# Kernel tuning notes

Hardware: AMD Instinct MI355X
Metric: run time of the kernel (lower is better)

Reference implementation:

```python
import jax, jax.numpy as jnp
import numpy as np

PATCH_LEN = 25
RATIO = 0.1
B, C, T = 128, 128, 5000
NUM_PATCHES = T // PATCH_LEN          # 200
TOTAL_UNITS = C * NUM_PATCHES         # 25600
NUM_MASK = int(TOTAL_UNITS * RATIO)   # 2560


def setup_inputs() -> dict:
    key = jax.random.key(0)
    kx, kp = jax.random.split(key)
    x = jax.random.normal(kx, (B, C, T), dtype=jnp.float32)
    # torch.randperm(total_units)[:num_mask] -> unique unit indices
    idx = jax.random.permutation(kp, TOTAL_UNITS)[:NUM_MASK].astype(jnp.int32)
    return {"x": x, "idx": idx}


def reference(x, idx):
    # Fused mask-generate-and-multiply: one scatter + one elementwise multiply
    # instead of num_mask separate slice-assign kernels.
    Bx, Cx, Tx = x.shape
    num_patches = Tx // PATCH_LEN
    # unit mask over (C * num_patches): 0 at masked units, 1 elsewhere
    unit_mask = jnp.ones((Cx * num_patches,), dtype=x.dtype).at[idx].set(0.0)
    # expand each unit to its patch_len samples -> (C, T)
    mask = jnp.repeat(unit_mask.reshape(Cx, num_patches), PATCH_LEN, axis=1)
    return x * mask[None, :, :]
```

## Files before the change

kernel.cpp:

```cpp
#include <hip/hip_runtime.h>


#define PM_B 128
#define PM_C 128
#define PM_T 5000
#define PM_PATCH 25
#define PM_NP 200
#define PM_UNITS (PM_C * PM_NP)
#define PM_NMASK 2560

__global__ void pm_init_mask(float* __restrict__ um) {
    int i = blockIdx.x * blockDim.x + threadIdx.x;
    if (i < PM_UNITS) um[i] = 1.0f;
}

__global__ void pm_scatter_mask(const int* __restrict__ idx, float* __restrict__ um) {
    int i = blockIdx.x * blockDim.x + threadIdx.x;
    if (i < PM_NMASK) um[idx[i]] = 0.0f;
}

__global__ __launch_bounds__(256) void pm_apply_mask(
    const float* __restrict__ x,
    const float* __restrict__ um,
    float* __restrict__ out)
{
    const int c  = blockIdx.y;
    const int b  = blockIdx.z;
    const int t0 = (blockIdx.x * blockDim.x + threadIdx.x) * 4;
    if (t0 >= PM_T) return;

    const float* __restrict__ um_c = um + c * PM_NP;
    const size_t base = ((size_t)b * PM_C + c) * PM_T + t0;

    float4 v = *reinterpret_cast<const float4*>(x + base);

    const int p0 = t0 / PM_PATCH;
    const int p3 = (t0 + 3) / PM_PATCH;
    const float m0 = um_c[p0];
    if (p0 == p3) {
        v.x *= m0; v.y *= m0; v.z *= m0; v.w *= m0;
    } else {
        const float m3 = um_c[p3];
        const int boundary = p3 * PM_PATCH;
        v.x *= (t0 + 0 < boundary) ? m0 : m3;
        v.y *= (t0 + 1 < boundary) ? m0 : m3;
        v.z *= (t0 + 2 < boundary) ? m0 : m3;
        v.w *= (t0 + 3 < boundary) ? m0 : m3;
    }

    *reinterpret_cast<float4*>(out + base) = v;
}

extern "C" void kernel_launch(void* const* d_in, const int* in_sizes, int n_in,
                              void* d_out, int out_size, void* d_ws, size_t ws_size,
                              hipStream_t stream) {
    const float* x   = (const float*)d_in[0];
    const int*   idx = (const int*)d_in[1];
    float*       out = (float*)d_out;
    float*       um  = (float*)d_ws;

    pm_init_mask<<<(PM_UNITS + 255) / 256, 256, 0, stream>>>(um);
    pm_scatter_mask<<<(PM_NMASK + 255) / 256, 256, 0, stream>>>(idx, um);

    dim3 grid((PM_T / 4 + 255) / 256, PM_C, PM_B);
    pm_apply_mask<<<grid, 256, 0, stream>>>(x, um, out);
}
```

Measured before the change: 124.1 us.

## Use grid-stride flat loop with nontemporal loads/stores and memset-based inverted mask

Replaces the 3D grid with a flat grid-stride loop over all float4 elements on 2048 blocks, and uses nontemporal loads and stores for the streaming x/out traffic. The init kernel is replaced by hipMemsetAsync with an inverted mask (scatter writes 1, apply uses 1-m). This targets the partially idle blocks of the old grid (1250 float4 per row over 1280 threads), launch overhead, and cache pollution. The per-element row division and the grid-stride loop add some integer work.

Measured after the change: 125.0 us, median of 2. About the same (+0.8%).

```diff
diff --git a/kernel.cpp b/kernel.cpp
--- a/kernel.cpp
+++ b/kernel.cpp
@@ -8,47 +8,46 @@
 #define PM_NP 200
 #define PM_UNITS (PM_C * PM_NP)
 #define PM_NMASK 2560
+#define PM_F4_PER_ROW (PM_T / 4)
+#define PM_F4_TOTAL (PM_B * PM_C * PM_F4_PER_ROW)
 
-__global__ void pm_init_mask(float* __restrict__ um) {
-    int i = blockIdx.x * blockDim.x + threadIdx.x;
-    if (i < PM_UNITS) um[i] = 1.0f;
-}
+typedef float f32x4 __attribute__((ext_vector_type(4)));
 
 __global__ void pm_scatter_mask(const int* __restrict__ idx, float* __restrict__ um) {
     int i = blockIdx.x * blockDim.x + threadIdx.x;
-    if (i < PM_NMASK) um[idx[i]] = 0.0f;
+    if (i < PM_NMASK) um[idx[i]] = 1.0f;
 }
 
 __global__ __launch_bounds__(256) void pm_apply_mask(
-    const float* __restrict__ x,
+    const f32x4* __restrict__ x,
     const float* __restrict__ um,
-    float* __restrict__ out)
+    f32x4* __restrict__ out)
 {
-    const int c  = blockIdx.y;
-    const int b  = blockIdx.z;
-    const int t0 = (blockIdx.x * blockDim.x + threadIdx.x) * 4;
-    if (t0 >= PM_T) return;
+    unsigned i = blockIdx.x * 256u + threadIdx.x;
+    const unsigned stride = gridDim.x * 256u;
+    for (; i < PM_F4_TOTAL; i += stride) {
+        const unsigned row = i / PM_F4_PER_ROW;
+        const unsigned t0  = (i - row * PM_F4_PER_ROW) * 4u;
+        const float* __restrict__ um_c = um + (row & (PM_C - 1)) * PM_NP;
 
-    const float* __restrict__ um_c = um + c * PM_NP;
-    const size_t base = ((size_t)b * PM_C + c) * PM_T + t0;
+        f32x4 v = __builtin_nontemporal_load(x + i);
 
-    float4 v = *reinterpret_cast<const float4*>(x + base);
+        const unsigned p0 = t0 / PM_PATCH;
+        const unsigned p3 = (t0 + 3u) / PM_PATCH;
+        const float m0 = 1.0f - um_c[p0];
+        if (p0 == p3) {
+            v *= m0;
+        } else {
+            const float m3 = 1.0f - um_c[p3];
+            const unsigned boundary = p3 * PM_PATCH;
+            v.x *= (t0 + 0u < boundary) ? m0 : m3;
+            v.y *= (t0 + 1u < boundary) ? m0 : m3;
+            v.z *= (t0 + 2u < boundary) ? m0 : m3;
+            v.w *= (t0 + 3u < boundary) ? m0 : m3;
+        }
 
-    const int p0 = t0 / PM_PATCH;
-    const int p3 = (t0 + 3) / PM_PATCH;
-    const float m0 = um_c[p0];
-    if (p0 == p3) {
-        v.x *= m0; v.y *= m0; v.z *= m0; v.w *= m0;
-    } else {
-        const float m3 = um_c[p3];
-        const int boundary = p3 * PM_PATCH;
-        v.x *= (t0 + 0 < boundary) ? m0 : m3;
-        v.y *= (t0 + 1 < boundary) ? m0 : m3;
-        v.z *= (t0 + 2 < boundary) ? m0 : m3;
-        v.w *= (t0 + 3 < boundary) ? m0 : m3;
+        __builtin_nontemporal_store(v, out + i);
     }
-
-    *reinterpret_cast<float4*>(out + base) = v;
 }
 
 extern "C" void kernel_launch(void* const* d_in, const int* in_sizes, int n_in,
@@ -59,9 +58,9 @@
     float*       out = (float*)d_out;
     float*       um  = (float*)d_ws;
 
-    pm_init_mask<<<(PM_UNITS + 255) / 256, 256, 0, stream>>>(um);
+    (void)hipMemsetAsync(um, 0, PM_UNITS * sizeof(float), stream);
     pm_scatter_mask<<<(PM_NMASK + 255) / 256, 256, 0, stream>>>(idx, um);
 
-    dim3 grid((PM_T / 4 + 255) / 256, PM_C, PM_B);
-    pm_apply_mask<<<grid, 256, 0, stream>>>(x, um, out);
+    pm_apply_mask<<<2048, 256, 0, stream>>>(
+        (const f32x4*)x, um, (f32x4*)out);
 }
```

## Replace mask-multiply with device copy plus sparse zeroing of masked patches

Applied to the files above, without the earlier changes.

Drops the unit-mask build and the full elementwise multiply kernels. Instead it copies x to out with a device-to-device async memcpy, then launches one kernel that writes zeros only to the masked patches (2560 units × 128 batches × 25 samples). The aim is to cut the launch count and the per-element mask logic. In exchange it adds a second pass of scattered 25-float writes on top of a full-bandwidth copy. It also sets masked elements to 0 rather than x*0, so non-finite inputs would no longer give NaN.

Measured after the change: 161.7 us. 30.3% more time.

```diff
diff --git a/kernel.cpp b/kernel.cpp
--- a/kernel.cpp
+++ b/kernel.cpp
@@ -6,49 +6,28 @@
 #define PM_T 5000
 #define PM_PATCH 25
 #define PM_NP 200
-#define PM_UNITS (PM_C * PM_NP)
 #define PM_NMASK 2560
+#define PM_ZERO_PER_UNIT (PM_B * PM_PATCH)
+#define PM_ZERO_TOTAL (PM_NMASK * PM_ZERO_PER_UNIT)
 
-__global__ void pm_init_mask(float* __restrict__ um) {
-    int i = blockIdx.x * blockDim.x + threadIdx.x;
-    if (i < PM_UNITS) um[i] = 1.0f;
-}
-
-__global__ void pm_scatter_mask(const int* __restrict__ idx, float* __restrict__ um) {
-    int i = blockIdx.x * blockDim.x + threadIdx.x;
-    if (i < PM_NMASK) um[idx[i]] = 0.0f;
-}
-
-__global__ __launch_bounds__(256) void pm_apply_mask(
-    const float* __restrict__ x,
-    const float* __restrict__ um,
+__global__ __launch_bounds__(256) void pm_zero_patches(
+    const int* __restrict__ idx,
     float* __restrict__ out)
 {
-    const int c  = blockIdx.y;
-    const int b  = blockIdx.z;
-    const int t0 = (blockIdx.x * blockDim.x + threadIdx.x) * 4;
-    if (t0 >= PM_T) return;
+    unsigned n = blockIdx.x * 256u + threadIdx.x;
+    if (n >= PM_ZERO_TOTAL) return;
 
-    const float* __restrict__ um_c = um + c * PM_NP;
-    const size_t base = ((size_t)b * PM_C + c) * PM_T + t0;
+    const unsigned j = n / PM_ZERO_PER_UNIT;
+    const unsigned r = n - j * PM_ZERO_PER_UNIT;
+    const unsigned b = r / PM_PATCH;
+    const unsigned s = r - b * PM_PATCH;
 
-    float4 v = *reinterpret_cast<const float4*>(x + base);
+    const unsigned u = (unsigned)idx[j];
+    const unsigned c = u / PM_NP;
+    const unsigned p = u - c * PM_NP;
 
-    const int p0 = t0 / PM_PATCH;
-    const int p3 = (t0 + 3) / PM_PATCH;
-    const float m0 = um_c[p0];
-    if (p0 == p3) {
-        v.x *= m0; v.y *= m0; v.z *= m0; v.w *= m0;
-    } else {
-        const float m3 = um_c[p3];
-        const int boundary = p3 * PM_PATCH;
-        v.x *= (t0 + 0 < boundary) ? m0 : m3;
-        v.y *= (t0 + 1 < boundary) ? m0 : m3;
-        v.z *= (t0 + 2 < boundary) ? m0 : m3;
-        v.w *= (t0 + 3 < boundary) ? m0 : m3;
-    }
-
-    *reinterpret_cast<float4*>(out + base) = v;
+    const size_t t = (size_t)p * PM_PATCH + s;
+    out[((size_t)b * PM_C + c) * PM_T + t] = 0.0f;
 }
 
 extern "C" void kernel_launch(void* const* d_in, const int* in_sizes, int n_in,
@@ -57,11 +36,10 @@
     const float* x   = (const float*)d_in[0];
     const int*   idx = (const int*)d_in[1];
     float*       out = (float*)d_out;
-    float*       um  = (float*)d_ws;
 
-    pm_init_mask<<<(PM_UNITS + 255) / 256, 256, 0, stream>>>(um);
-    pm_scatter_mask<<<(PM_NMASK + 255) / 256, 256, 0, stream>>>(idx, um);
+    (void)hipMemcpyAsync(out, x, (size_t)out_size * sizeof(float),
+                         hipMemcpyDeviceToDevice, stream);
 
-    dim3 grid((PM_T / 4 + 255) / 256, PM_C, PM_B);
-    pm_apply_mask<<<grid, 256, 0, stream>>>(x, um, out);
+    const unsigned blocks = (PM_ZERO_TOTAL + 255u) / 256u;
+    pm_zero_patches<<<blocks, 256, 0, stream>>>(idx, out);
 }
```
